# Optimization experiments

Hardware: AMD Instinct MI355X
Metric: run time of the kernel (lower is better)

The kernel has to match this reference:

```python
import jax, jax.numpy as jnp
import numpy as np

N = 10000      # nodes
E = 80000      # edges
D = 128        # d_model
H = 8          # num_heads
DH = 128       # d_head
DFF = 512      # d_ff
CLAMP = 5.0
EPS = 1e-5


def setup_inputs() -> dict:
    key = jax.random.key(0)
    ks = jax.random.split(key, 10)
    s = 0.05
    return {
        "feat": jax.random.normal(ks[0], (N, D), jnp.float32),
        "src": jax.random.randint(ks[1], (E,), 0, N),
        "dst": jax.random.randint(ks[2], (E,), 0, N),
        # projections stored as (in, out); x @ W == torch Linear(bias=False)
        "Wq": jax.random.normal(ks[3], (D, H * DH), jnp.float32) * s,
        "Wk": jax.random.normal(ks[4], (D, H * DH), jnp.float32) * s,
        "Wv": jax.random.normal(ks[5], (D, H * DH), jnp.float32) * s,
        "Wo": jax.random.normal(ks[6], (H * DH, D), jnp.float32) * s,
        "g1": jnp.ones((D,), jnp.float32),
        "b1": jnp.zeros((D,), jnp.float32),
        "W1": jax.random.normal(ks[7], (D, DFF), jnp.float32) * s,
        "bf1": jnp.zeros((DFF,), jnp.float32),
        "W2": jax.random.normal(ks[8], (DFF, D), jnp.float32) * s,
        "bf2": jnp.zeros((D,), jnp.float32),
        "g2": jnp.ones((D,), jnp.float32),
        "b2": jnp.zeros((D,), jnp.float32),
    }


def _layer_norm(x, g, b):
    mu = x.mean(-1, keepdims=True)
    xc = x - mu
    var = (xc * xc).mean(-1, keepdims=True)
    return xc * jax.lax.rsqrt(var + EPS) * g + b


def reference(feat, src, dst, Wq, Wk, Wv, Wo, g1, b1, W1, bf1, W2, bf2, g2, b2):
    h_src = feat[src]                              # (E, D) gather
    h_dst = feat[dst]                              # (E, D)
    q = (h_dst @ Wq).reshape(E, H, DH)             # query from destination node
    k = (h_src @ Wk).reshape(E, H, DH)
    v = (h_src @ Wv).reshape(E, H, DH)
    # per-edge logits: QK dot per head, scale, clamp
    u = jnp.clip((q * k).sum(-1) / np.sqrt(DH), -CLAMP, CLAMP)  # (E, H)
    # edge_softmax over incoming edges of each destination node
    m = jax.ops.segment_max(u, dst, num_segments=N)             # (N, H)
    ex = jnp.exp(u - m[dst])
    den = jax.ops.segment_sum(ex, dst, num_segments=N)          # (N, H)
    a = ex / den[dst]                                           # (E, H)
    # weighted V, segment-sum to destination nodes
    agg = jax.ops.segment_sum(a[..., None] * v, dst, num_segments=N)  # (N, H, DH)
    uh = _layer_norm(feat + agg.reshape(N, H * DH) @ Wo, g1, b1)
    ffn = jax.nn.relu(uh @ W1 + bf1) @ W2 + bf2
    return _layer_norm(uh + ffn, g2, b2)
```

## Files before the change

### kernel.cpp

```cpp
#include <hip/hip_runtime.h>

typedef unsigned int uint;
typedef unsigned short ushort;
typedef __attribute__((ext_vector_type(8))) short short8;
typedef __attribute__((ext_vector_type(4))) float f32x4;

#define DEV static __device__ __forceinline__

DEV float bf_lo(uint v) { return __uint_as_float(v << 16); }
DEV float bf_hi(uint v) { return __uint_as_float(v & 0xffff0000u); }
DEV ushort f2bf(float f) {
    uint u = __float_as_uint(f);
    u += 0x7fffu + ((u >> 16) & 1u);
    return (ushort)(u >> 16);
}
DEV void stC(float* p, float v) { *p = v; }
DEV void stC(ushort* p, float v) { *p = f2bf(v); }

#define DPPADD(v, ctrl) \
    ((v) + __int_as_float(__builtin_amdgcn_mov_dpp(__float_as_int(v), (ctrl), 0xF, 0xF, true)))

DEV void gload16(const void* gsrc, void* ldst)
{
    __builtin_amdgcn_global_load_lds(
        (__attribute__((address_space(1))) void*)const_cast<void*>(gsrc),
        (__attribute__((address_space(3))) void*)ldst,
        16, 0, 0);
}

template <typename OT>
DEV void transp_body(float (*tile)[65], const float* __restrict__ in,
                     OT* __restrict__ out, int R, int C, int bid, int t)
{
    const int nbx = C >> 6;
    const int bx = bid % nbx, by = bid / nbx;
#pragma unroll
    for (int it = 0; it < 4; ++it) {
        int idx = it * 256 + t;
        int rr = idx >> 4, cc4 = (idx & 15) * 4;
        float4 v = *reinterpret_cast<const float4*>(in + (size_t)(by * 64 + rr) * C + bx * 64 + cc4);
        tile[cc4][rr] = v.x; tile[cc4 + 1][rr] = v.y;
        tile[cc4 + 2][rr] = v.z; tile[cc4 + 3][rr] = v.w;
    }
    __syncthreads();
#pragma unroll
    for (int it = 0; it < 4; ++it) {
        int idx = it * 256 + t;
        int cc = idx >> 4, rr4 = (idx & 15) * 4;
        OT* po = out + (size_t)(bx * 64 + cc) * R + by * 64 + rr4;
        if constexpr (__is_same(OT, float)) {
            float4 o = { tile[cc][rr4], tile[cc][rr4 + 1], tile[cc][rr4 + 2], tile[cc][rr4 + 3] };
            *reinterpret_cast<float4*>(po) = o;
        } else {
            ushort4 o = { f2bf(tile[cc][rr4]), f2bf(tile[cc][rr4 + 1]),
                          f2bf(tile[cc][rr4 + 2]), f2bf(tile[cc][rr4 + 3]) };
            *reinterpret_cast<ushort4*>(po) = o;
        }
    }
}

__global__ __launch_bounds__(256) void prep1_kernel(
    int4* __restrict__ cntd4, int nz,
    const float* __restrict__ feat, ushort* __restrict__ featbf,
    const float* __restrict__ Wo, float* __restrict__ WoT,
    const float* __restrict__ W1, ushort* __restrict__ W1T,
    const float* __restrict__ W2, ushort* __restrict__ W2T, int N)
{
    __shared__ float tile[64][65];
    const int zb = (nz + 255) / 256;
    const int nf = (N * 32 + 255) / 256;
    const int b = blockIdx.x, t = threadIdx.x;
    if (b < zb) {
        int i = b * 256 + t;
        if (i < nz) cntd4[i] = int4{0, 0, 0, 0};
    } else if (b < zb + nf) {
        int i = (b - zb) * 256 + t;
        if (i >= N * 32) return;
        float4 v = reinterpret_cast<const float4*>(feat)[i];
        ushort4 o;
        o.x = f2bf(v.x); o.y = f2bf(v.y); o.z = f2bf(v.z); o.w = f2bf(v.w);
        reinterpret_cast<ushort4*>(featbf)[i] = o;
    } else if (b < zb + nf + 32) {
        transp_body<float>(tile, Wo, WoT, 1024, 128, b - zb - nf, t);
    } else if (b < zb + nf + 48) {
        transp_body<ushort>(tile, W1, W1T, 128, 512, b - zb - nf - 32, t);
    } else {
        transp_body<ushort>(tile, W2, W2T, 512, 128, b - zb - nf - 48, t);
    }
}

__global__ __launch_bounds__(256) void hist_mpt_kernel(
    const int* __restrict__ dst, int* __restrict__ cntd, int E, int eb,
    const float* __restrict__ Wq, const float* __restrict__ Wk,
    const float* __restrict__ Wv, const float* __restrict__ WoT,
    ushort* __restrict__ MPT)
{
    __shared__ char lds[65536];
    const int b = blockIdx.x, t = threadIdx.x;
    if (b < eb) {
        int e = b * 256 + t;
        if (e < E) atomicAdd(&cntd[dst[e]], 1);
        return;
    }
    char* As = lds;
    char* Bs = lds + 32768;

    const int mb = b - eb;
    const int part = mb >> 3, h = mb & 7;
    const int lane = t & 63, w = t >> 6;
    const int frow = lane & 15, kgrp = lane >> 4;

    const float* Asrc = part ? WoT : Wk;
    const float* Bsrc = part ? Wv : Wq;
    const float ascale = part ? 1.f : 0.08838834764831845f;

#pragma unroll
    for (int it = 0; it < 16; ++it) {
        int idx = it * 256 + t;
        int r = idx >> 5, c4 = (idx & 31) * 4;
        size_t goff = (size_t)r * 1024 + h * 128 + c4;
        float4 va = *reinterpret_cast<const float4*>(Asrc + goff);
        ushort4 ua = { f2bf(va.x * ascale), f2bf(va.y * ascale),
                       f2bf(va.z * ascale), f2bf(va.w * ascale) };
        *reinterpret_cast<ushort4*>(&As[r * 256 + ((c4 * 2) ^ ((r & 7) << 4))]) = ua;
        float4 vb = *reinterpret_cast<const float4*>(Bsrc + goff);
        ushort4 ub = { f2bf(vb.x), f2bf(vb.y), f2bf(vb.z), f2bf(vb.w) };
        *reinterpret_cast<ushort4*>(&Bs[r * 256 + ((c4 * 2) ^ ((r & 7) << 4))]) = ub;
    }
    __syncthreads();

    f32x4 acc[2][8] = {};
#pragma unroll
    for (int ks = 0; ks < 4; ++ks) {
        int koff = ks * 64 + kgrp * 16;
        short8 bfr[8];
#pragma unroll
        for (int fn = 0; fn < 8; ++fn) {
            int col = fn * 16 + frow;
            bfr[fn] = *reinterpret_cast<const short8*>(&Bs[col * 256 + (koff ^ ((col & 7) << 4))]);
        }
#pragma unroll
        for (int fm = 0; fm < 2; ++fm) {
            int row = w * 32 + fm * 16 + frow;
            short8 a = *reinterpret_cast<const short8*>(&As[row * 256 + (koff ^ ((row & 7) << 4))]);
#pragma unroll
            for (int fn = 0; fn < 8; ++fn)
                acc[fm][fn] = __builtin_amdgcn_mfma_f32_16x16x32_bf16(a, bfr[fn], acc[fm][fn], 0, 0, 0);
        }
    }

    const size_t base = ((size_t)part * 1024 + h * 128) * 128;
#pragma unroll
    for (int fm = 0; fm < 2; ++fm)
#pragma unroll
        for (int fn = 0; fn < 8; ++fn)
#pragma unroll
            for (int r = 0; r < 4; ++r) {
                int j = w * 32 + fm * 16 + kgrp * 4 + r;
                int i = fn * 16 + frow;
                MPT[base + (size_t)j * 128 + i] = f2bf(acc[fm][fn][r]);
            }
}

__global__ __launch_bounds__(1024) void scan1_kernel(
    const int* __restrict__ cntd, int* __restrict__ offd, int* __restrict__ curd, int N)
{
    __shared__ int ls[1024];
    const int t = threadIdx.x;
    const int chunk = (N + 1023) >> 10;
    int base = t * chunk;
    int s = 0;
    for (int i = 0; i < chunk; ++i) {
        int idx = base + i;
        if (idx < N) s += cntd[idx];
    }
    ls[t] = s;
    __syncthreads();
    for (int d = 1; d < 1024; d <<= 1) {
        int v = (t >= d) ? ls[t - d] : 0;
        __syncthreads();
        ls[t] += v;
        __syncthreads();
    }
    int run = t ? ls[t - 1] : 0;
    for (int i = 0; i < chunk; ++i) {
        int idx = base + i;
        if (idx < N) {
            offd[idx] = run;
            curd[idx] = run;
            run += cntd[idx];
        }
    }
    if (t == 1023) offd[N] = run;
}

__global__ __launch_bounds__(256) void gvo_scat_kernel(
    const ushort* __restrict__ A, const ushort* __restrict__ BT,
    ushort* __restrict__ C, int M, int nbg,
    const int* __restrict__ src, const int* __restrict__ dst,
    int* __restrict__ curd, int* __restrict__ src_d, int* __restrict__ dst_d, int E)
{
    __shared__ char lds[32768];
    const int b = blockIdx.x, t = threadIdx.x;

    if (b >= nbg) {
        int e = (b - nbg) * 256 + t;
        if (e >= E) return;
        int s = src[e], d = dst[e];
        int pd = atomicAdd(&curd[d], 1);
        src_d[pd] = s;
        dst_d[pd] = d;
        return;
    }

    char* AsB = lds;
    char* BsB = lds + 16384;
    const int m0 = (b >> 4) * 128;
    const int n0 = (b & 15) * 128;
    const int lane = t & 63, wid = t >> 6;
    const int wm = wid >> 1, wn = wid & 1;
    const int frow = lane & 15, kgrp = lane >> 4;
    const int wub = (t & 192) * 16;

    f32x4 acc[4][4] = {};

    for (int kk = 0; kk < 128; kk += 64) {
#pragma unroll
        for (int it = 0; it < 4; ++it) {
            int q = it * 256 + t;
            int r = q >> 3;
            int swz = ((q & 7) * 16) ^ ((r & 7) << 4);
            gload16((const char*)A + ((size_t)(m0 + r) * 128 + kk) * 2 + swz,
                    AsB + it * 4096 + wub);
        }
#pragma unroll
        for (int it = 0; it < 4; ++it) {
            int q = it * 256 + t;
            int r = q >> 3;
            int swz = ((q & 7) * 16) ^ ((r & 7) << 4);
            gload16((const char*)BT + ((size_t)(n0 + r) * 128 + kk) * 2 + swz,
                    BsB + it * 4096 + wub);
        }
        __syncthreads();
#pragma unroll
        for (int kp = 0; kp < 2; ++kp) {
            const int koffb = kp * 64 + kgrp * 16;
            short8 bb[4];
#pragma unroll
            for (int fn = 0; fn < 4; ++fn) {
                int col = wn * 64 + fn * 16 + frow;
                bb[fn] = *reinterpret_cast<const short8*>(&BsB[col * 128 + (koffb ^ ((col & 7) << 4))]);
            }
#pragma unroll
            for (int fm = 0; fm < 4; ++fm) {
                int row = wm * 64 + fm * 16 + frow;
                short8 a = *reinterpret_cast<const short8*>(&AsB[row * 128 + (koffb ^ ((row & 7) << 4))]);
#pragma unroll
                for (int fn = 0; fn < 4; ++fn)
                    acc[fm][fn] = __builtin_amdgcn_mfma_f32_16x16x32_bf16(a, bb[fn], acc[fm][fn], 0, 0, 0);
            }
        }
        __syncthreads();
    }

#pragma unroll
    for (int fm = 0; fm < 4; ++fm)
#pragma unroll
        for (int fn = 0; fn < 4; ++fn)
#pragma unroll
            for (int r = 0; r < 4; ++r) {
                int gm = m0 + wm * 64 + fm * 16 + kgrp * 4 + r;
                int gn = n0 + wn * 64 + fn * 16 + frow;
                if (gm >= M) continue;
                stC(&C[(size_t)gm * 2048 + gn], acc[fm][fn][r]);
            }
}

__global__ __launch_bounds__(256) void edge_fused_kernel(
    const ushort* __restrict__ featbf, const ushort* __restrict__ GVO,
    const int* __restrict__ src_d, const int* __restrict__ dst_d,
    const int* __restrict__ offd, float* __restrict__ exws,
    const float* __restrict__ feat, const float* __restrict__ g1,
    const float* __restrict__ b1, float* __restrict__ uh,
    ushort* __restrict__ uhbf, int N)
{
    const int d0 = blockIdx.x * 4;
    const int t = threadIdx.x;
    const int blo = offd[d0];
    const int bhi = offd[min(d0 + 4, N)];

    {
        int g = t >> 4, li = t & 15;
        for (int p = blo + g; p < bhi; p += 16) {
            int s = src_d[p], d = dst_d[p];
            uint4 f = reinterpret_cast<const uint4*>(featbf)[(size_t)s * 16 + li];
            const uint4* Grow = reinterpret_cast<const uint4*>(GVO) + (size_t)d * 256 + li;
            float sel = 0.f;
#pragma unroll
            for (int h = 0; h < 8; ++h) {
                uint4 gv = Grow[h * 16];
                float pv = bf_lo(gv.x) * bf_lo(f.x) + bf_hi(gv.x) * bf_hi(f.x);
                pv += bf_lo(gv.y) * bf_lo(f.y) + bf_hi(gv.y) * bf_hi(f.y);
                pv += bf_lo(gv.z) * bf_lo(f.z) + bf_hi(gv.z) * bf_hi(f.z);
                pv += bf_lo(gv.w) * bf_lo(f.w) + bf_hi(gv.w) * bf_hi(f.w);
                pv = DPPADD(pv, 0xB1);
                pv = DPPADD(pv, 0x4E);
                pv = DPPADD(pv, 0x141);
                pv = DPPADD(pv, 0x128);
                sel = (li == h) ? pv : sel;
            }
            float u = fminf(fmaxf(sel, -5.f), 5.f);
            float ex = __expf(u);
            if (li < 8) exws[(size_t)p * 8 + li] = ex;
        }
    }
    __threadfence_block();
    __syncthreads();

    const int lane = t & 63;
    const int d = d0 + (t >> 6);
    if (d >= N) return;
    const int lo = offd[d], hi = offd[d + 1];

    int h = lane & 7;
    float den = 0.f;
    for (int i = lo + (lane >> 3); i < hi; i += 8)
        den += exws[(size_t)i * 8 + h];
    den += __shfl_xor(den, 8);
    den += __shfl_xor(den, 16);
    den += __shfl_xor(den, 32);
    float rh = 1.f / den;
    float rv0 = __shfl(rh, 0), rv1 = __shfl(rh, 1), rv2 = __shfl(rh, 2), rv3 = __shfl(rh, 3);
    float rv4 = __shfl(rh, 4), rv5 = __shfl(rh, 5), rv6 = __shfl(rh, 6), rv7 = __shfl(rh, 7);

    float acc0 = 0.f, acc1 = 0.f;
    uint cg0 = 0, cg1 = 0, cg2 = 0, cg3 = 0, cg4 = 0, cg5 = 0, cg6 = 0, cg7 = 0;
    float4 ce0 = {}, ce1 = {};
    if (lo < hi) {
        int s0 = src_d[lo];
        const uint* vr = reinterpret_cast<const uint*>(GVO + (size_t)s0 * 2048 + 1024);
        cg0 = vr[lane];       cg1 = vr[64 + lane];  cg2 = vr[128 + lane]; cg3 = vr[192 + lane];
        cg4 = vr[256 + lane]; cg5 = vr[320 + lane]; cg6 = vr[384 + lane]; cg7 = vr[448 + lane];
        ce0 = *reinterpret_cast<const float4*>(&exws[(size_t)lo * 8]);
        ce1 = *reinterpret_cast<const float4*>(&exws[(size_t)lo * 8 + 4]);
    }
    for (int i = lo; i < hi; ++i) {
        uint ng0 = 0, ng1 = 0, ng2 = 0, ng3 = 0, ng4 = 0, ng5 = 0, ng6 = 0, ng7 = 0;
        float4 ne0 = {}, ne1 = {};
        if (i + 1 < hi) {
            int sn = src_d[i + 1];
            const uint* vr = reinterpret_cast<const uint*>(GVO + (size_t)sn * 2048 + 1024);
            ng0 = vr[lane];       ng1 = vr[64 + lane];  ng2 = vr[128 + lane]; ng3 = vr[192 + lane];
            ng4 = vr[256 + lane]; ng5 = vr[320 + lane]; ng6 = vr[384 + lane]; ng7 = vr[448 + lane];
            ne0 = *reinterpret_cast<const float4*>(&exws[(size_t)(i + 1) * 8]);
            ne1 = *reinterpret_cast<const float4*>(&exws[(size_t)(i + 1) * 8 + 4]);
        }
        float a0 = ce0.x * rv0, a1 = ce0.y * rv1, a2 = ce0.z * rv2, a3 = ce0.w * rv3;
        float a4 = ce1.x * rv4, a5 = ce1.y * rv5, a6 = ce1.z * rv6, a7 = ce1.w * rv7;
        acc0 += a0 * bf_lo(cg0) + a1 * bf_lo(cg1) + a2 * bf_lo(cg2) + a3 * bf_lo(cg3)
              + a4 * bf_lo(cg4) + a5 * bf_lo(cg5) + a6 * bf_lo(cg6) + a7 * bf_lo(cg7);
        acc1 += a0 * bf_hi(cg0) + a1 * bf_hi(cg1) + a2 * bf_hi(cg2) + a3 * bf_hi(cg3)
              + a4 * bf_hi(cg4) + a5 * bf_hi(cg5) + a6 * bf_hi(cg6) + a7 * bf_hi(cg7);
        cg0 = ng0; cg1 = ng1; cg2 = ng2; cg3 = ng3;
        cg4 = ng4; cg5 = ng5; cg6 = ng6; cg7 = ng7;
        ce0 = ne0; ce1 = ne1;
    }

    float2 v = reinterpret_cast<const float2*>(feat)[(size_t)d * 64 + lane];
    v.x += acc0;
    v.y += acc1;
    float sum = v.x + v.y;
#pragma unroll
    for (int off = 32; off; off >>= 1) sum += __shfl_xor(sum, off);
    float mean = sum * (1.f / 128.f);
    float cx = v.x - mean, cy = v.y - mean;
    float vs = cx * cx + cy * cy;
#pragma unroll
    for (int off = 32; off; off >>= 1) vs += __shfl_xor(vs, off);
    float r = rsqrtf(vs * (1.f / 128.f) + 1e-5f);
    float2 gg = reinterpret_cast<const float2*>(g1)[lane];
    float2 bb = reinterpret_cast<const float2*>(b1)[lane];
    float2 o;
    o.x = cx * r * gg.x + bb.x;
    o.y = cy * r * gg.y + bb.y;
    reinterpret_cast<float2*>(uh)[(size_t)d * 64 + lane] = o;
    ushort2 ob; ob.x = f2bf(o.x); ob.y = f2bf(o.y);
    reinterpret_cast<ushort2*>(uhbf)[(size_t)d * 64 + lane] = ob;
}

template <int NTILE, typename OT, bool BIAS, bool RELU, bool RES>
__global__ __launch_bounds__(256) void gemm_mfma(
    const ushort* __restrict__ A, const ushort* __restrict__ BT,
    const float* __restrict__ bias, const float* __restrict__ res,
    OT* __restrict__ C, int M, int K, int NC)
{
    constexpr int FN = NTILE * 2;
    constexpr int WN = NTILE * 32;
    __shared__ char lds[16384 + NTILE * 8192];
    char* AsB = lds;
    char* BsB = lds + 16384;

    const int m0 = blockIdx.y * 128;
    const int n0 = blockIdx.x * (NTILE * 64);
    const int t = threadIdx.x;
    const int lane = t & 63, wid = t >> 6;
    const int wm = wid >> 1, wn = wid & 1;
    const int frow = lane & 15, kgrp = lane >> 4;
    const int wub = (t & 192) * 16;

    f32x4 acc[4][FN] = {};

    for (int kk = 0; kk < K; kk += 64) {
#pragma unroll
        for (int it = 0; it < 4; ++it) {
            int q = it * 256 + t;
            int r = q >> 3;
            int swz = ((q & 7) * 16) ^ ((r & 7) << 4);
            gload16((const char*)A + ((size_t)(m0 + r) * K + kk) * 2 + swz,
                    AsB + it * 4096 + wub);
        }
#pragma unroll
        for (int it = 0; it < 2 * NTILE; ++it) {
            int q = it * 256 + t;
            int r = q >> 3;
            int swz = ((q & 7) * 16) ^ ((r & 7) << 4);
            gload16((const char*)BT + ((size_t)(n0 + r) * K + kk) * 2 + swz,
                    BsB + it * 4096 + wub);
        }
        __syncthreads();
#pragma unroll
        for (int kp = 0; kp < 2; ++kp) {
            const int koffb = kp * 64 + kgrp * 16;
            short8 b[FN];
#pragma unroll
            for (int fn = 0; fn < FN; ++fn) {
                int col = wn * WN + fn * 16 + frow;
                b[fn] = *reinterpret_cast<const short8*>(&BsB[col * 128 + (koffb ^ ((col & 7) << 4))]);
            }
#pragma unroll
            for (int fm = 0; fm < 4; ++fm) {
                int row = wm * 64 + fm * 16 + frow;
                short8 a = *reinterpret_cast<const short8*>(&AsB[row * 128 + (koffb ^ ((row & 7) << 4))]);
#pragma unroll
                for (int fn = 0; fn < FN; ++fn)
                    acc[fm][fn] = __builtin_amdgcn_mfma_f32_16x16x32_bf16(a, b[fn], acc[fm][fn], 0, 0, 0);
            }
        }
        __syncthreads();
    }

#pragma unroll
    for (int fm = 0; fm < 4; ++fm)
#pragma unroll
        for (int fn = 0; fn < FN; ++fn)
#pragma unroll
            for (int r = 0; r < 4; ++r) {
                int gm = m0 + wm * 64 + fm * 16 + kgrp * 4 + r;
                int gn = n0 + wn * WN + fn * 16 + frow;
                if (gm >= M) continue;
                float v = acc[fm][fn][r];
                if (BIAS) v += bias[gn];
                if (RELU) v = fmaxf(v, 0.f);
                if (RES) v += res[(size_t)gm * NC + gn];
                stC(&C[(size_t)gm * NC + gn], v);
            }
}

__global__ __launch_bounds__(256) void gemm_mfma64(
    const ushort* __restrict__ A, const ushort* __restrict__ BT,
    const float* __restrict__ bias, const float* __restrict__ res,
    float* __restrict__ C, int M, int K, int NC)
{
    __shared__ char lds[16384];
    char* AsB = lds;
    char* BsB = lds + 8192;

    const int m0 = blockIdx.y * 64;
    const int n0 = blockIdx.x * 64;
    const int t = threadIdx.x;
    const int lane = t & 63, wid = t >> 6;
    const int wm = wid >> 1, wn = wid & 1;
    const int frow = lane & 15, kgrp = lane >> 4;
    const int wub = (t & 192) * 16;

    f32x4 acc[2][2] = {};

    for (int kk = 0; kk < K; kk += 64) {
#pragma unroll
        for (int it = 0; it < 2; ++it) {
            int q = it * 256 + t;
            int r = q >> 3;
            int swz = ((q & 7) * 16) ^ ((r & 7) << 4);
            gload16((const char*)A + ((size_t)(m0 + r) * K + kk) * 2 + swz,
                    AsB + it * 4096 + wub);
        }
#pragma unroll
        for (int it = 0; it < 2; ++it) {
            int q = it * 256 + t;
            int r = q >> 3;
            int swz = ((q & 7) * 16) ^ ((r & 7) << 4);
            gload16((const char*)BT + ((size_t)(n0 + r) * K + kk) * 2 + swz,
                    BsB + it * 4096 + wub);
        }
        __syncthreads();
#pragma unroll
        for (int kp = 0; kp < 2; ++kp) {
            const int koffb = kp * 64 + kgrp * 16;
            short8 b[2];
#pragma unroll
            for (int fn = 0; fn < 2; ++fn) {
                int col = wn * 32 + fn * 16 + frow;
                b[fn] = *reinterpret_cast<const short8*>(&BsB[col * 128 + (koffb ^ ((col & 7) << 4))]);
            }
#pragma unroll
            for (int fm = 0; fm < 2; ++fm) {
                int row = wm * 32 + fm * 16 + frow;
                short8 a = *reinterpret_cast<const short8*>(&AsB[row * 128 + (koffb ^ ((row & 7) << 4))]);
#pragma unroll
                for (int fn = 0; fn < 2; ++fn)
                    acc[fm][fn] = __builtin_amdgcn_mfma_f32_16x16x32_bf16(a, b[fn], acc[fm][fn], 0, 0, 0);
            }
        }
        __syncthreads();
    }

#pragma unroll
    for (int fm = 0; fm < 2; ++fm)
#pragma unroll
        for (int fn = 0; fn < 2; ++fn)
#pragma unroll
            for (int r = 0; r < 4; ++r) {
                int gm = m0 + wm * 32 + fm * 16 + kgrp * 4 + r;
                int gn = n0 + wn * 32 + fn * 16 + frow;
                if (gm >= M) continue;
                float v = acc[fm][fn][r] + bias[gn] + res[(size_t)gm * NC + gn];
                C[(size_t)gm * NC + gn] = v;
            }
}

__global__ __launch_bounds__(256) void ln_kernel(
    const float* __restrict__ x, const float* __restrict__ g,
    const float* __restrict__ b, float* __restrict__ out, int M)
{
    int row = (int)((blockIdx.x * 256 + threadIdx.x) >> 6);
    int lane = threadIdx.x & 63;
    if (row >= M) return;
    float2 v = reinterpret_cast<const float2*>(x)[(size_t)row * 64 + lane];
    float sum = v.x + v.y;
#pragma unroll
    for (int off = 32; off; off >>= 1) sum += __shfl_xor(sum, off);
    float mean = sum * (1.f / 128.f);
    float cx = v.x - mean, cy = v.y - mean;
    float vs = cx * cx + cy * cy;
#pragma unroll
    for (int off = 32; off; off >>= 1) vs += __shfl_xor(vs, off);
    float r = rsqrtf(vs * (1.f / 128.f) + 1e-5f);
    float2 gg = reinterpret_cast<const float2*>(g)[lane];
    float2 bb = reinterpret_cast<const float2*>(b)[lane];
    float2 o;
    o.x = cx * r * gg.x + bb.x;
    o.y = cy * r * gg.y + bb.y;
    reinterpret_cast<float2*>(out)[(size_t)row * 64 + lane] = o;
}

extern "C" void kernel_launch(void* const* d_in, const int* in_sizes, int n_in,
                              void* d_out, int out_size, void* d_ws, size_t ws_size,
                              hipStream_t stream)
{
    const float* feat = (const float*)d_in[0];
    const int*   src  = (const int*)d_in[1];
    const int*   dst  = (const int*)d_in[2];
    const float* Wq   = (const float*)d_in[3];
    const float* Wk   = (const float*)d_in[4];
    const float* Wv   = (const float*)d_in[5];
    const float* Wo   = (const float*)d_in[6];
    const float* g1   = (const float*)d_in[7];
    const float* b1   = (const float*)d_in[8];
    const float* W1   = (const float*)d_in[9];
    const float* bf1  = (const float*)d_in[10];
    const float* W2   = (const float*)d_in[11];
    const float* bf2  = (const float*)d_in[12];
    const float* g2   = (const float*)d_in[13];
    const float* b2   = (const float*)d_in[14];
    const int N = in_sizes[0] / 128;
    const int E = in_sizes[1];
    float* out = (float*)d_out;

    char* w = (char*)d_ws;
    auto alloc = [&](size_t bytes) {
        char* p = w;
        w += (bytes + 255) & ~(size_t)255;
        return p;
    };
    ushort* MPT    = (ushort*)alloc((size_t)2048 * 128 * 2);
    float*  WoT    = (float*)alloc((size_t)128 * 1024 * 4);
    ushort* W1T    = (ushort*)alloc((size_t)512 * 128 * 2);
    ushort* W2T    = (ushort*)alloc((size_t)128 * 512 * 2);
    ushort* featbf = (ushort*)alloc((size_t)N * 128 * 2);
    ushort* GVO    = (ushort*)alloc((size_t)N * 2048 * 2);
    float*  exws   = (float*)alloc((size_t)E * 8 * 4);
    int*    cntd   = (int*)alloc((size_t)((N + 3) & ~3) * 4);
    int*    offd   = (int*)alloc((size_t)(N + 1) * 4);
    int*    curd   = (int*)alloc((size_t)N * 4);
    int*    src_d  = (int*)alloc((size_t)E * 4);
    int*    dst_d  = (int*)alloc((size_t)E * 4);
    float*  uh     = (float*)alloc((size_t)N * 128 * 4);
    ushort* uhbf   = (ushort*)alloc((size_t)N * 128 * 2);
    ushort* f1     = (ushort*)alloc((size_t)N * 512 * 2);
    float*  pre2   = (float*)alloc((size_t)N * 128 * 4);

    int nz = (N + 3) / 4;
    int zb = (nz + 255) / 256;
    int nf = (N * 32 + 255) / 256;
    prep1_kernel<<<zb + nf + 64, 256, 0, stream>>>(
        (int4*)cntd, nz, feat, featbf, Wo, WoT, W1, W1T, W2, W2T, N);

    int eb = (E + 255) / 256;
    hist_mpt_kernel<<<eb + 16, 256, 0, stream>>>(
        dst, cntd, E, eb, Wq, Wk, Wv, WoT, MPT);

    scan1_kernel<<<1, 1024, 0, stream>>>(cntd, offd, curd, N);

    int nbg = 16 * ((N + 127) / 128);
    gvo_scat_kernel<<<nbg + eb, 256, 0, stream>>>(
        featbf, MPT, GVO, N, nbg, src, dst, curd, src_d, dst_d, E);

    edge_fused_kernel<<<(N + 3) / 4, 256, 0, stream>>>(
        featbf, GVO, src_d, dst_d, offd, exws, feat, g1, b1, uh, uhbf, N);

    dim3 f1_grid(512 / 128, (N + 127) / 128);
    gemm_mfma<2, ushort, true, true, false><<<f1_grid, 256, 0, stream>>>(
        uhbf, W1T, bf1, nullptr, f1, N, 128, 512);
    dim3 f2_grid(128 / 64, (N + 63) / 64);
    gemm_mfma64<<<f2_grid, 256, 0, stream>>>(
        f1, W2T, bf2, uh, pre2, N, 512, 128);
    int nwaves_n = (N * 64 + 255) / 256;
    ln_kernel<<<nwaves_n, 256, 0, stream>>>(pre2, g2, b2, out, N);
}
```

Before: 124.2 us.

## Split edge aggregation into source-sorted weighting and destination-sorted sum passes

Adds a second CSR ordering of edges by source node, using a second histogram, scan and scatter. Normalised attention weights are written back to the edge buffer. A new kernel then walks edges in source order and computes the per-edge weighted V vector (summed over heads), so GVO rows are read with locality. The result is written to a bf16 per-edge buffer in destination order. A final kernel sums these per destination and applies LayerNorm. This trades the scattered per-destination GVO gathers for extra atomics, extra kernels, and an E×128 bf16 intermediate written and read back, plus bf16 rounding of per-edge messages.

Result: slower. 145.5 us (+17.1%).

```diff
diff --git a/kernel.cpp b/kernel.cpp
--- a/kernel.cpp
+++ b/kernel.cpp
@@ -60,7 +60,7 @@
 }
 
 __global__ __launch_bounds__(256) void prep1_kernel(
-    int4* __restrict__ cntd4, int nz,
+    int4* __restrict__ cnt4, int nz,
     const float* __restrict__ feat, ushort* __restrict__ featbf,
     const float* __restrict__ Wo, float* __restrict__ WoT,
     const float* __restrict__ W1, ushort* __restrict__ W1T,
@@ -72,7 +72,7 @@
     const int b = blockIdx.x, t = threadIdx.x;
     if (b < zb) {
         int i = b * 256 + t;
-        if (i < nz) cntd4[i] = int4{0, 0, 0, 0};
+        if (i < nz) cnt4[i] = int4{0, 0, 0, 0};
     } else if (b < zb + nf) {
         int i = (b - zb) * 256 + t;
         if (i >= N * 32) return;
@@ -90,7 +90,8 @@
 }
 
 __global__ __launch_bounds__(256) void hist_mpt_kernel(
-    const int* __restrict__ dst, int* __restrict__ cntd, int E, int eb,
+    const int* __restrict__ src, const int* __restrict__ dst,
+    int* __restrict__ cnts, int* __restrict__ cntd, int E, int eb,
     const float* __restrict__ Wq, const float* __restrict__ Wk,
     const float* __restrict__ Wv, const float* __restrict__ WoT,
     ushort* __restrict__ MPT)
@@ -99,7 +100,10 @@
     const int b = blockIdx.x, t = threadIdx.x;
     if (b < eb) {
         int e = b * 256 + t;
-        if (e < E) atomicAdd(&cntd[dst[e]], 1);
+        if (e < E) {
+            atomicAdd(&cnts[src[e]], 1);
+            atomicAdd(&cntd[dst[e]], 1);
+        }
         return;
     }
     char* As = lds;
@@ -162,43 +166,52 @@
             }
 }
 
-__global__ __launch_bounds__(1024) void scan1_kernel(
-    const int* __restrict__ cntd, int* __restrict__ offd, int* __restrict__ curd, int N)
+__global__ __launch_bounds__(1024) void scan2_kernel(
+    const int* __restrict__ cnts, const int* __restrict__ cntd,
+    int* __restrict__ offd, int* __restrict__ curs, int* __restrict__ curd, int N)
 {
     __shared__ int ls[1024];
     const int t = threadIdx.x;
     const int chunk = (N + 1023) >> 10;
-    int base = t * chunk;
-    int s = 0;
-    for (int i = 0; i < chunk; ++i) {
-        int idx = base + i;
-        if (idx < N) s += cntd[idx];
-    }
-    ls[t] = s;
-    __syncthreads();
-    for (int d = 1; d < 1024; d <<= 1) {
-        int v = (t >= d) ? ls[t - d] : 0;
-        __syncthreads();
-        ls[t] += v;
-        __syncthreads();
-    }
-    int run = t ? ls[t - 1] : 0;
-    for (int i = 0; i < chunk; ++i) {
-        int idx = base + i;
-        if (idx < N) {
-            offd[idx] = run;
-            curd[idx] = run;
-            run += cntd[idx];
-        }
-    }
-    if (t == 1023) offd[N] = run;
+#pragma unroll 1
+    for (int a = 0; a < 2; ++a) {
+        const int* in = a ? cntd : cnts;
+        int* cur = a ? curd : curs;
+        int base = t * chunk;
+        int s = 0;
+        for (int i = 0; i < chunk; ++i) {
+            int idx = base + i;
+            if (idx < N) s += in[idx];
+        }
+        ls[t] = s;
+        __syncthreads();
+        for (int d = 1; d < 1024; d <<= 1) {
+            int v = (t >= d) ? ls[t - d] : 0;
+            __syncthreads();
+            ls[t] += v;
+            __syncthreads();
+        }
+        int run = t ? ls[t - 1] : 0;
+        for (int i = 0; i < chunk; ++i) {
+            int idx = base + i;
+            if (idx < N) {
+                if (a) offd[idx] = run;
+                cur[idx] = run;
+                run += in[idx];
+            }
+        }
+        if (a && t == 1023) offd[N] = run;
+        __syncthreads();
+    }
 }
 
 __global__ __launch_bounds__(256) void gvo_scat_kernel(
     const ushort* __restrict__ A, const ushort* __restrict__ BT,
     ushort* __restrict__ C, int M, int nbg,
     const int* __restrict__ src, const int* __restrict__ dst,
-    int* __restrict__ curd, int* __restrict__ src_d, int* __restrict__ dst_d, int E)
+    int* __restrict__ curs, int* __restrict__ curd,
+    int* __restrict__ src_d, int* __restrict__ dst_d,
+    int* __restrict__ src_s, int* __restrict__ pd_s, int E)
 {
     __shared__ char lds[32768];
     const int b = blockIdx.x, t = threadIdx.x;
@@ -210,6 +223,9 @@
         int pd = atomicAdd(&curd[d], 1);
         src_d[pd] = s;
         dst_d[pd] = d;
+        int ps = atomicAdd(&curs[s], 1);
+        src_s[ps] = s;
+        pd_s[ps] = pd;
         return;
     }
 
@@ -276,13 +292,10 @@
             }
 }
 
-__global__ __launch_bounds__(256) void edge_fused_kernel(
+__global__ __launch_bounds__(256) void logits_den_kernel(
     const ushort* __restrict__ featbf, const ushort* __restrict__ GVO,
     const int* __restrict__ src_d, const int* __restrict__ dst_d,
-    const int* __restrict__ offd, float* __restrict__ exws,
-    const float* __restrict__ feat, const float* __restrict__ g1,
-    const float* __restrict__ b1, float* __restrict__ uh,
-    ushort* __restrict__ uhbf, int N)
+    const int* __restrict__ offd, float* __restrict__ exws, int N)
 {
     const int d0 = blockIdx.x * 4;
     const int t = threadIdx.x;
@@ -321,54 +334,57 @@
     const int d = d0 + (t >> 6);
     if (d >= N) return;
     const int lo = offd[d], hi = offd[d + 1];
-
-    int h = lane & 7;
+    int es = lane >> 3, h = lane & 7;
     float den = 0.f;
-    for (int i = lo + (lane >> 3); i < hi; i += 8)
+    for (int i = lo + es; i < hi; i += 8)
         den += exws[(size_t)i * 8 + h];
     den += __shfl_xor(den, 8);
     den += __shfl_xor(den, 16);
     den += __shfl_xor(den, 32);
-    float rh = 1.f / den;
-    float rv0 = __shfl(rh, 0), rv1 = __shfl(rh, 1), rv2 = __shfl(rh, 2), rv3 = __shfl(rh, 3);
-    float rv4 = __shfl(rh, 4), rv5 = __shfl(rh, 5), rv6 = __shfl(rh, 6), rv7 = __shfl(rh, 7);
-
+    float r = 1.f / den;
+    for (int i = lo + es; i < hi; i += 8)
+        exws[(size_t)i * 8 + h] *= r;
+}
+
+__global__ __launch_bounds__(256) void edge_w_kernel(
+    const ushort* __restrict__ GVO, const int* __restrict__ src_s,
+    const int* __restrict__ pd_s, const float* __restrict__ exws,
+    ushort* __restrict__ wbuf, int E)
+{
+    int q = (int)((blockIdx.x * 256 + threadIdx.x) >> 6);
+    int lane = threadIdx.x & 63;
+    if (q >= E) return;
+    int s = src_s[q];
+    int pd = pd_s[q];
+    float aval = (lane < 8) ? exws[(size_t)pd * 8 + lane] : 0.f;
     float acc0 = 0.f, acc1 = 0.f;
-    uint cg0 = 0, cg1 = 0, cg2 = 0, cg3 = 0, cg4 = 0, cg5 = 0, cg6 = 0, cg7 = 0;
-    float4 ce0 = {}, ce1 = {};
-    if (lo < hi) {
-        int s0 = src_d[lo];
-        const uint* vr = reinterpret_cast<const uint*>(GVO + (size_t)s0 * 2048 + 1024);
-        cg0 = vr[lane];       cg1 = vr[64 + lane];  cg2 = vr[128 + lane]; cg3 = vr[192 + lane];
-        cg4 = vr[256 + lane]; cg5 = vr[320 + lane]; cg6 = vr[384 + lane]; cg7 = vr[448 + lane];
-        ce0 = *reinterpret_cast<const float4*>(&exws[(size_t)lo * 8]);
-        ce1 = *reinterpret_cast<const float4*>(&exws[(size_t)lo * 8 + 4]);
-    }
+#pragma unroll
+    for (int h = 0; h < 8; ++h) {
+        float a = __shfl(aval, h);
+        uint gv = *reinterpret_cast<const uint*>(&GVO[(size_t)s * 2048 + 1024 + h * 128 + 2 * lane]);
+        acc0 += a * bf_lo(gv);
+        acc1 += a * bf_hi(gv);
+    }
+    ushort2 o; o.x = f2bf(acc0); o.y = f2bf(acc1);
+    reinterpret_cast<ushort2*>(wbuf)[(size_t)pd * 64 + lane] = o;
+}
+
+__global__ __launch_bounds__(256) void agg_ln1_kernel(
+    const ushort* __restrict__ wbuf, const int* __restrict__ offd,
+    const float* __restrict__ feat, const float* __restrict__ g1,
+    const float* __restrict__ b1, float* __restrict__ uh,
+    ushort* __restrict__ uhbf, int N)
+{
+    int d = (int)((blockIdx.x * 256 + threadIdx.x) >> 6);
+    int lane = threadIdx.x & 63;
+    if (d >= N) return;
+    float2 v = reinterpret_cast<const float2*>(feat)[(size_t)d * 64 + lane];
+    int lo = offd[d], hi = offd[d + 1];
     for (int i = lo; i < hi; ++i) {
-        uint ng0 = 0, ng1 = 0, ng2 = 0, ng3 = 0, ng4 = 0, ng5 = 0, ng6 = 0, ng7 = 0;
-        float4 ne0 = {}, ne1 = {};
-        if (i + 1 < hi) {
-            int sn = src_d[i + 1];
-            const uint* vr = reinterpret_cast<const uint*>(GVO + (size_t)sn * 2048 + 1024);
-            ng0 = vr[lane];       ng1 = vr[64 + lane];  ng2 = vr[128 + lane]; ng3 = vr[192 + lane];
-            ng4 = vr[256 + lane]; ng5 = vr[320 + lane]; ng6 = vr[384 + lane]; ng7 = vr[448 + lane];
-            ne0 = *reinterpret_cast<const float4*>(&exws[(size_t)(i + 1) * 8]);
-            ne1 = *reinterpret_cast<const float4*>(&exws[(size_t)(i + 1) * 8 + 4]);
-        }
-        float a0 = ce0.x * rv0, a1 = ce0.y * rv1, a2 = ce0.z * rv2, a3 = ce0.w * rv3;
-        float a4 = ce1.x * rv4, a5 = ce1.y * rv5, a6 = ce1.z * rv6, a7 = ce1.w * rv7;
-        acc0 += a0 * bf_lo(cg0) + a1 * bf_lo(cg1) + a2 * bf_lo(cg2) + a3 * bf_lo(cg3)
-              + a4 * bf_lo(cg4) + a5 * bf_lo(cg5) + a6 * bf_lo(cg6) + a7 * bf_lo(cg7);
-        acc1 += a0 * bf_hi(cg0) + a1 * bf_hi(cg1) + a2 * bf_hi(cg2) + a3 * bf_hi(cg3)
-              + a4 * bf_hi(cg4) + a5 * bf_hi(cg5) + a6 * bf_hi(cg6) + a7 * bf_hi(cg7);
-        cg0 = ng0; cg1 = ng1; cg2 = ng2; cg3 = ng3;
-        cg4 = ng4; cg5 = ng5; cg6 = ng6; cg7 = ng7;
-        ce0 = ne0; ce1 = ne1;
-    }
-
-    float2 v = reinterpret_cast<const float2*>(feat)[(size_t)d * 64 + lane];
-    v.x += acc0;
-    v.y += acc1;
+        uint wv = reinterpret_cast<const uint*>(wbuf)[(size_t)i * 64 + lane];
+        v.x += bf_lo(wv);
+        v.y += bf_hi(wv);
+    }
     float sum = v.x + v.y;
 #pragma unroll
     for (int off = 32; off; off >>= 1) sum += __shfl_xor(sum, off);
@@ -599,34 +615,48 @@
     ushort* featbf = (ushort*)alloc((size_t)N * 128 * 2);
     ushort* GVO    = (ushort*)alloc((size_t)N * 2048 * 2);
     float*  exws   = (float*)alloc((size_t)E * 8 * 4);
-    int*    cntd   = (int*)alloc((size_t)((N + 3) & ~3) * 4);
+    int*    cnt2   = (int*)alloc((size_t)((2 * N + 3) & ~3) * 4);
+    int*    cnts   = cnt2;
+    int*    cntd   = cnt2 + N;
     int*    offd   = (int*)alloc((size_t)(N + 1) * 4);
+    int*    curs   = (int*)alloc((size_t)N * 4);
     int*    curd   = (int*)alloc((size_t)N * 4);
     int*    src_d  = (int*)alloc((size_t)E * 4);
     int*    dst_d  = (int*)alloc((size_t)E * 4);
+    int*    src_s  = (int*)alloc((size_t)E * 4);
+    int*    pd_s   = (int*)alloc((size_t)E * 4);
+    ushort* wbuf   = (ushort*)alloc((size_t)E * 128 * 2);
     float*  uh     = (float*)alloc((size_t)N * 128 * 4);
     ushort* uhbf   = (ushort*)alloc((size_t)N * 128 * 2);
     ushort* f1     = (ushort*)alloc((size_t)N * 512 * 2);
     float*  pre2   = (float*)alloc((size_t)N * 128 * 4);
 
-    int nz = (N + 3) / 4;
+    int nz = (2 * N + 3) / 4;
     int zb = (nz + 255) / 256;
     int nf = (N * 32 + 255) / 256;
     prep1_kernel<<<zb + nf + 64, 256, 0, stream>>>(
-        (int4*)cntd, nz, feat, featbf, Wo, WoT, W1, W1T, W2, W2T, N);
+        (int4*)cnt2, nz, feat, featbf, Wo, WoT, W1, W1T, W2, W2T, N);
 
     int eb = (E + 255) / 256;
     hist_mpt_kernel<<<eb + 16, 256, 0, stream>>>(
-        dst, cntd, E, eb, Wq, Wk, Wv, WoT, MPT);
-
-    scan1_kernel<<<1, 1024, 0, stream>>>(cntd, offd, curd, N);
+        src, dst, cnts, cntd, E, eb, Wq, Wk, Wv, WoT, MPT);
+
+    scan2_kernel<<<1, 1024, 0, stream>>>(cnts, cntd, offd, curs, curd, N);
 
     int nbg = 16 * ((N + 127) / 128);
     gvo_scat_kernel<<<nbg + eb, 256, 0, stream>>>(
-        featbf, MPT, GVO, N, nbg, src, dst, curd, src_d, dst_d, E);
-
-    edge_fused_kernel<<<(N + 3) / 4, 256, 0, stream>>>(
-        featbf, GVO, src_d, dst_d, offd, exws, feat, g1, b1, uh, uhbf, N);
+        featbf, MPT, GVO, N, nbg, src, dst, curs, curd,
+        src_d, dst_d, src_s, pd_s, E);
+
+    logits_den_kernel<<<(N + 3) / 4, 256, 0, stream>>>(
+        featbf, GVO, src_d, dst_d, offd, exws, N);
+
+    edge_w_kernel<<<(E + 3) / 4, 256, 0, stream>>>(
+        GVO, src_s, pd_s, exws, wbuf, E);
+
+    int nwaves_n = (N * 64 + 255) / 256;
+    agg_ln1_kernel<<<nwaves_n, 256, 0, stream>>>(
+        wbuf, offd, feat, g1, b1, uh, uhbf, N);
 
     dim3 f1_grid(512 / 128, (N + 127) / 128);
     gemm_mfma<2, ushort, true, true, false><<<f1_grid, 256, 0, stream>>>(
@@ -634,6 +664,5 @@
     dim3 f2_grid(128 / 64, (N + 63) / 64);
     gemm_mfma64<<<f2_grid, 256, 0, stream>>>(
         f1, W2T, bf2, uh, pre2, N, 512, 128);
-    int nwaves_n = (N * 64 + 255) / 256;
     ln_kernel<<<nwaves_n, 256, 0, stream>>>(pre2, g2, b2, out, N);
 }
```
